# Performance work log

Measured on AMD Instinct MI355X. Metric: run time of the kernel, lower is better.

## Reference

```python
import math
import jax, jax.numpy as jnp
import numpy as np

B, S, D, H = 2, 2048, 1024, 16
HD = D // H  # 64


def setup_inputs() -> dict:
    key = jax.random.key(0)
    k = jax.random.split(key, 8)
    x = jax.random.normal(k[0], (B, S, D), dtype=jnp.float32)
    # RoPE tables: inv_freq over half dim, emb = concat(freqs, freqs)
    inv_freq = 1.0 / (10000.0 ** (jnp.arange(0, HD, 2, dtype=jnp.float32) / HD))
    pos = jnp.arange(S, dtype=jnp.float32)
    freqs = pos[:, None] * inv_freq[None, :]            # [S, HD/2]
    emb = jnp.concatenate([freqs, freqs], axis=-1)      # [S, HD]
    cos = jnp.cos(emb)[:, None, :]                      # [S, 1, HD] broadcasts over [B,S,H,HD]
    sin = jnp.sin(emb)[:, None, :]
    # causal additive mask [1, 1, S, S]
    neg = jnp.finfo(jnp.float32).min
    mask = jnp.where(jnp.tril(jnp.ones((S, S), dtype=bool)), 0.0, neg)[None, None]
    scale = 0.02
    wq = jax.random.normal(k[1], (D, D), dtype=jnp.float32) * scale
    wk = jax.random.normal(k[2], (D, D), dtype=jnp.float32) * scale
    wv = jax.random.normal(k[3], (D, D), dtype=jnp.float32) * scale
    wo = jax.random.normal(k[4], (D, D), dtype=jnp.float32) * scale
    return {"x": x, "cos": cos, "sin": sin, "mask": mask,
            "wq": wq, "wk": wk, "wv": wv, "wo": wo}


def rotate_half(t):
    t1, t2 = t[..., : t.shape[-1] // 2], t[..., t.shape[-1] // 2:]
    return jnp.concatenate([-t2, t1], axis=-1)


def reference(x, cos, sin, mask, wq, wk, wv, wo):
    b, s, d = x.shape
    # torch nn.Linear: y = x @ W^T  (W is [out, in])
    q = (x @ wq.T).reshape(b, s, H, HD)
    kk = (x @ wk.T).reshape(b, s, H, HD)
    v = (x @ wv.T).reshape(b, s, H, HD)
    q = q * cos + rotate_half(q) * sin
    kk = kk * cos + rotate_half(kk) * sin
    q = q.transpose(0, 2, 1, 3)   # [b, h, s, hd]
    kk = kk.transpose(0, 2, 1, 3)
    v = v.transpose(0, 2, 1, 3)
    scores = jnp.einsum('bhqd,bhkd->bhqk', q, kk) / math.sqrt(HD)
    scores = scores + mask
    probs = jax.nn.softmax(scores.astype(jnp.float32), axis=-1).astype(q.dtype)
    out = jnp.einsum('bhqk,bhkd->bhqd', probs, v)
    out = out.transpose(0, 2, 1, 3).reshape(b, s, d)
    return out @ wo.T
```

## Files before the change

### kernel.cpp

```cpp
#include <hip/hip_runtime.h>
#include <hip/hip_bf16.h>

typedef __hip_bfloat16 bf16;
typedef unsigned short u16;
typedef __attribute__((ext_vector_type(8))) short short8;
typedef __attribute__((ext_vector_type(4))) float floatx4;

constexpr int B_ = 2, S_ = 2048, D_ = 1024, H_ = 16, HD_ = 64;
constexpr int QT = 64, KT = 64, PAD = 72;
constexpr int NQT = S_ / QT;
constexpr int GK = 1024;

__device__ inline float b2f(u16 u) {
    union { unsigned int i; float f; } v; v.i = ((unsigned int)u) << 16; return v.f;
}
__device__ inline u16 f2b(float f) {
    bf16 h = __float2bfloat16(f); return *(u16*)&h;
}

__device__ inline void gl16(const u16* g, u16* l) {
    __builtin_amdgcn_global_load_lds(
        (const __attribute__((address_space(1))) unsigned int*)g,
        (__attribute__((address_space(3))) unsigned int*)l, 16, 0, 0);
}

__global__ __launch_bounds__(256) void cvt_kernel(
    const float* __restrict__ x,  const float* __restrict__ wq,
    const float* __restrict__ wk, const float* __restrict__ wv,
    const float* __restrict__ wo,
    u16* __restrict__ Xb, u16* __restrict__ Wb)
{
    const size_t c = (size_t)blockIdx.x * 256 + threadIdx.x;
    const float* src; u16* dst; size_t off;
    if (c < (size_t)(1 << 19)) { src = x; dst = Xb; off = c; }
    else {
        const size_t w = c - (1 << 19);
        const int wi = (int)(w >> 17);
        off = w & ((1 << 17) - 1);
        src = (wi == 0) ? wq : (wi == 1) ? wk : (wi == 2) ? wv : wo;
        dst = Wb + ((size_t)wi << 20);
    }
    const float4 a = *(const float4*)(src + off * 8);
    const float4 b = *(const float4*)(src + off * 8 + 4);
    ushort4 u0; u0.x = f2b(a.x); u0.y = f2b(a.y); u0.z = f2b(a.z); u0.w = f2b(a.w);
    ushort4 u1; u1.x = f2b(b.x); u1.y = f2b(b.y); u1.z = f2b(b.z); u1.w = f2b(b.w);
    *(ushort4*)(dst + off * 8)     = u0;
    *(ushort4*)(dst + off * 8 + 4) = u1;
}

template <int NW, int ROPE, typename TC>
__global__ __launch_bounds__(256) void gemm_fused(
    const u16* __restrict__ A, const u16* __restrict__ Wb,
    const float* __restrict__ cosp, const float* __restrict__ sinp,
    TC* __restrict__ C0, TC* __restrict__ C1, TC* __restrict__ C2)
{
    constexpr int AS_E = 128 * 32;
    constexpr int BS_E = NW * 64 * 32;
    __shared__ __align__(16) u16 As[2][AS_E];
    __shared__ __align__(16) u16 Bs[2][BS_E];

    const int bid = blockIdx.x;
    const int xcd = bid & 7, idx = bid >> 3;
    const int y = xcd * 4 + (idx & 3);
    const int x = idx >> 2;

    const int tid = threadIdx.x;
    const int wave = tid >> 6, lane = tid & 63;
    const int quad = lane >> 4, l16 = lane & 15;
    const int wm = wave >> 1, wn = wave & 1;
    const int m0 = y * 128, n0 = x * 64;

    const int srw = lane >> 2;
    const int scn = (lane & 3) ^ (srw & 3);

    floatx4 acc[4][NW][2] = {};

    auto stage = [&](int k0, int bufi) {
#pragma unroll
        for (int j = 0; j < 2; ++j) {
            const int rb = wave * 32 + j * 16;
            gl16(A + (size_t)(m0 + rb + srw) * GK + k0 + scn * 8, &As[bufi][rb * 32]);
        }
        if (NW == 3) {
#pragma unroll
            for (int j = 0; j < 3; ++j) {
                const int rb = wave * 48 + j * 16;
                const int w  = rb >> 6, rin = rb & 63;
                gl16(Wb + ((size_t)w << 20) + (size_t)(n0 + rin + srw) * GK + k0 + scn * 8,
                     &Bs[bufi][rb * 32]);
            }
        } else {
            const int rb = wave * 16;
            gl16(Wb + (size_t)(n0 + rb + srw) * GK + k0 + scn * 8, &Bs[bufi][rb * 32]);
        }
    };

    stage(0, 0);
    for (int it = 0; it < 32; ++it) {
        __syncthreads();
        if (it + 1 < 32) stage((it + 1) * 32, (it + 1) & 1);
        const int cur = it & 1;

        short8 af[4];
#pragma unroll
        for (int mt = 0; mt < 4; ++mt) {
            const int R = wm * 64 + mt * 16 + l16;
            af[mt] = *(const short8*)&As[cur][R * 32 + ((quad ^ (R & 3)) * 8)];
        }
        short8 bfr[NW][2];
#pragma unroll
        for (int w = 0; w < NW; ++w)
#pragma unroll
            for (int nt = 0; nt < 2; ++nt) {
                const int Rb = w * 64 + nt * 32 + wn * 16 + l16;
                bfr[w][nt] = *(const short8*)&Bs[cur][Rb * 32 + ((quad ^ (Rb & 3)) * 8)];
            }
#pragma unroll
        for (int mt = 0; mt < 4; ++mt)
#pragma unroll
            for (int w = 0; w < NW; ++w)
#pragma unroll
                for (int nt = 0; nt < 2; ++nt)
                    acc[mt][w][nt] = __builtin_amdgcn_mfma_f32_16x16x32_bf16(
                        af[mt], bfr[w][nt], acc[mt][w][nt], 0, 0, 0);
    }

    if (ROPE) {
        float* Cs = (float*)&As[0][0];
        float* Sn = (float*)&Bs[0][0];
        const int s0 = m0 & (S_ - 1), bq = m0 >> 11, h = x;
        __syncthreads();
        {
            const int rr = tid >> 1;
            const int cc = (tid & 1) * 16;
            const float4* cp = (const float4*)(cosp + (size_t)(s0 + rr) * HD_ + cc);
            const float4* sp = (const float4*)(sinp + (size_t)(s0 + rr) * HD_ + cc);
            float4* cd = (float4*)&Cs[rr * 32 + cc];
            float4* sd = (float4*)&Sn[rr * 32 + cc];
            cd[0] = cp[0]; cd[1] = cp[1]; cd[2] = cp[2]; cd[3] = cp[3];
            sd[0] = sp[0]; sd[1] = sp[1]; sd[2] = sp[2]; sd[3] = sp[3];
        }
        __syncthreads();

        const float QSC = 0.125f * 1.44269504f;
        const int dlo = wn * 16 + l16;
        const int bh  = bq * H_ + h;
#pragma unroll
        for (int mt = 0; mt < 4; ++mt) {
#pragma unroll
            for (int r = 0; r < 4; ++r) {
                const int sr = wm * 64 + mt * 16 + quad * 4 + r;
                const float c1 = Cs[sr * 32 + dlo];
                const float s1 = Sn[sr * 32 + dlo];
                const size_t base = ((size_t)bh * S_ + s0 + sr) << 6;
                const float q0 = acc[mt][0][0][r], q1 = acc[mt][0][1][r];
                ((bf16*)C0)[base + dlo]      = __float2bfloat16((q0 * c1 - q1 * s1) * QSC);
                ((bf16*)C0)[base + dlo + 32] = __float2bfloat16((q1 * c1 + q0 * s1) * QSC);
                const float k0v = acc[mt][1][0][r], k1v = acc[mt][1][1][r];
                ((bf16*)C1)[base + dlo]      = __float2bfloat16(k0v * c1 - k1v * s1);
                ((bf16*)C1)[base + dlo + 32] = __float2bfloat16(k1v * c1 + k0v * s1);
            }
#pragma unroll
            for (int nt = 0; nt < 2; ++nt) {
                const int d  = nt * 32 + dlo;
                const int sb = (m0 & (S_ - 1)) + wm * 64 + mt * 16 + quad * 4;
                ushort4 pk;
                pk.x = f2b(acc[mt][2][nt][0]); pk.y = f2b(acc[mt][2][nt][1]);
                pk.z = f2b(acc[mt][2][nt][2]); pk.w = f2b(acc[mt][2][nt][3]);
                *(ushort4*)&((u16*)C2)[((size_t)(bh * HD_ + d) << 11) + sb] = pk;
            }
        }
    } else {
#pragma unroll
        for (int mt = 0; mt < 4; ++mt)
#pragma unroll
            for (int nt = 0; nt < 2; ++nt) {
                const int n = n0 + nt * 32 + wn * 16 + l16;
#pragma unroll
                for (int r = 0; r < 4; ++r) {
                    const int m = m0 + wm * 64 + mt * 16 + quad * 4 + r;
                    ((float*)C0)[(size_t)m * D_ + n] = acc[mt][0][nt][r];
                }
            }
    }
}

__global__ __launch_bounds__(256) void fa_kernel(
    const u16* __restrict__ Qg, const u16* __restrict__ Kg, const u16* __restrict__ Vt,
    bf16* __restrict__ Og)
{
    __shared__ __align__(16) u16 Kt[2][KT * PAD];
    __shared__ __align__(16) u16 Vs[2][HD_ * PAD];
    __shared__ __align__(16) u16 Pt[4 * 16 * PAD];

    const int flat = blockIdx.x;
    const int bx = flat >> 5;
    const int bh = flat & 31;
    const int b  = bh >> 4, h = bh & 15;
    const int tid  = threadIdx.x;
    const int wave = tid >> 6, lane = tid & 63;
    const int quad = lane >> 4, l16 = lane & 15;
    const int srow = tid >> 2, scol = (tid & 3) * 16;

    for (int half = 0; half < 2; ++half) {
        const int qt = half ? (NQT - 1 - bx) : bx;
        const int qb = qt * QT;

        const u16* qrow = Qg + ((size_t)bh * S_ + qb + wave * 16 + l16) * HD_;
        const short8 aq0 = *(const short8*)(qrow + quad * 8);
        const short8 aq1 = *(const short8*)(qrow + 32 + quad * 8);

        floatx4 oacc[4] = {{0,0,0,0},{0,0,0,0},{0,0,0,0},{0,0,0,0}};
        float lsum = 0.f;

        __syncthreads();
        {
            const u16* kp = Kg + ((size_t)bh * S_ + srow) * HD_ + scol;
            *(short8*)&Kt[0][srow * PAD + scol]     = *(const short8*)kp;
            *(short8*)&Kt[0][srow * PAD + scol + 8] = *(const short8*)(kp + 8);
            const u16* vp = Vt + ((size_t)bh * HD_ + srow) * S_ + scol;
            *(short8*)&Vs[0][srow * PAD + scol]     = *(const short8*)vp;
            *(short8*)&Vs[0][srow * PAD + scol + 8] = *(const short8*)(vp + 8);
        }
        __syncthreads();

        for (int it = 0; it <= qt; ++it) {
            const int  cur = it & 1;
            const bool pf  = (it < qt);
            short8 nk0, nk1, nv0, nv1;
            if (pf) {
                const int kb = (it + 1) * KT;
                const u16* kp = Kg + ((size_t)bh * S_ + kb + srow) * HD_ + scol;
                nk0 = *(const short8*)kp; nk1 = *(const short8*)(kp + 8);
                const u16* vp = Vt + ((size_t)bh * HD_ + srow) * S_ + kb + scol;
                nv0 = *(const short8*)vp; nv1 = *(const short8*)(vp + 8);
            }

            floatx4 sacc[4] = {{0,0,0,0},{0,0,0,0},{0,0,0,0},{0,0,0,0}};
#pragma unroll
            for (int kt = 0; kt < 4; ++kt) {
                const short8 bk0 = *(const short8*)&Kt[cur][(kt * 16 + l16) * PAD + quad * 8];
                const short8 bk1 = *(const short8*)&Kt[cur][(kt * 16 + l16) * PAD + 32 + quad * 8];
                sacc[kt] = __builtin_amdgcn_mfma_f32_16x16x32_bf16(bk0, aq0, sacc[kt], 0, 0, 0);
                sacc[kt] = __builtin_amdgcn_mfma_f32_16x16x32_bf16(bk1, aq1, sacc[kt], 0, 0, 0);
            }

            if (it == qt) {
                const int ql = wave * 16 + l16;
#pragma unroll
                for (int kt = 0; kt < 4; ++kt)
#pragma unroll
                    for (int r = 0; r < 4; ++r)
                        if (kt * 16 + quad * 4 + r > ql) sacc[kt][r] = -1.0e38f;
            }

            float rs = 0.f;
#pragma unroll
            for (int kt = 0; kt < 4; ++kt) {
                const float e0 = __builtin_amdgcn_exp2f(sacc[kt][0]);
                const float e1 = __builtin_amdgcn_exp2f(sacc[kt][1]);
                const float e2 = __builtin_amdgcn_exp2f(sacc[kt][2]);
                const float e3 = __builtin_amdgcn_exp2f(sacc[kt][3]);
                rs += (e0 + e1) + (e2 + e3);
                ushort4 pk; pk.x = f2b(e0); pk.y = f2b(e1); pk.z = f2b(e2); pk.w = f2b(e3);
                *(ushort4*)&Pt[(wave * 16 + l16) * PAD + kt * 16 + quad * 4] = pk;
            }
            rs += __shfl_xor(rs, 16);
            rs += __shfl_xor(rs, 32);
            lsum += rs;

            const short8 ap0 = *(const short8*)&Pt[(wave * 16 + l16) * PAD + quad * 8];
            const short8 ap1 = *(const short8*)&Pt[(wave * 16 + l16) * PAD + 32 + quad * 8];

#pragma unroll
            for (int dt = 0; dt < 4; ++dt) {
                const short8 bv0 = *(const short8*)&Vs[cur][(dt * 16 + l16) * PAD + quad * 8];
                const short8 bv1 = *(const short8*)&Vs[cur][(dt * 16 + l16) * PAD + 32 + quad * 8];
                oacc[dt] = __builtin_amdgcn_mfma_f32_16x16x32_bf16(bv0, ap0, oacc[dt], 0, 0, 0);
                oacc[dt] = __builtin_amdgcn_mfma_f32_16x16x32_bf16(bv1, ap1, oacc[dt], 0, 0, 0);
            }

            if (pf) {
                const int nb = cur ^ 1;
                *(short8*)&Kt[nb][srow * PAD + scol]     = nk0;
                *(short8*)&Kt[nb][srow * PAD + scol + 8] = nk1;
                *(short8*)&Vs[nb][srow * PAD + scol]     = nv0;
                *(short8*)&Vs[nb][srow * PAD + scol + 8] = nv1;
            }
            __syncthreads();
        }

        const float inv = 1.0f / lsum;
        bf16* orow = Og + ((size_t)(b * S_ + qb + wave * 16 + l16)) * D_ + h * HD_;
#pragma unroll
        for (int dt = 0; dt < 4; ++dt) {
            ushort4 pk;
            pk.x = f2b(oacc[dt][0] * inv);
            pk.y = f2b(oacc[dt][1] * inv);
            pk.z = f2b(oacc[dt][2] * inv);
            pk.w = f2b(oacc[dt][3] * inv);
            *(ushort4*)((u16*)orow + dt * 16 + quad * 4) = pk;
        }
    }
}

extern "C" void kernel_launch(void* const* d_in, const int* in_sizes, int n_in,
                              void* d_out, int out_size, void* d_ws, size_t ws_size,
                              hipStream_t stream)
{
    const float* x    = (const float*)d_in[0];
    const float* cosp = (const float*)d_in[1];
    const float* sinp = (const float*)d_in[2];
    const float* wq   = (const float*)d_in[4];
    const float* wk   = (const float*)d_in[5];
    const float* wv   = (const float*)d_in[6];
    const float* wo   = (const float*)d_in[7];
    float* out = (float*)d_out;

    u16* w0 = (u16*)d_ws;
    const size_t NE = (size_t)B_ * S_ * D_;
    u16* Qb  = w0;
    u16* Kb  = w0 + NE;
    u16* Vtb = w0 + 2 * NE;
    u16* Xb  = w0 + 3 * NE;
    u16* Wb  = w0 + 4 * NE;
    u16* Ab  = Xb;
    u16* Wob = Wb + 3 * (1 << 20);

    cvt_kernel<<<4096, 256, 0, stream>>>(x, wq, wk, wv, wo, Xb, Wb);

    gemm_fused<3, 1, bf16><<<512, 256, 0, stream>>>(
        Xb, Wb, cosp, sinp, (bf16*)Qb, (bf16*)Kb, (bf16*)Vtb);

    fa_kernel<<<dim3((NQT / 2) * 32, 1, 1), 256, 0, stream>>>(Qb, Kb, Vtb, (bf16*)Ab);

    gemm_fused<1, 0, float><<<512, 256, 0, stream>>>(
        Ab, Wob, cosp, sinp, out, out, out);
}
```

Measured before the change: 203.5 us.

## Split GEMM templates, load attention K/V from global, and retile output GEMM

The templated GEMM is split into a dedicated QKV kernel and a separate output-projection kernel. The output kernel uses a 64-wide K step with an XOR swizzle, single buffering, and a different XCD-aware block mapping. The attention kernel drops the shared-memory K/V staging and the paired causal half-tiles. Each block now handles one query tile, launched longest first, and every wave reads K and V fragments straight from global memory into registers, with K prefetched one step ahead. This removes LDS traffic and barriers, but each of the four waves reloads K/V from global or L2 on its own, and the single-buffered output GEMM exposes its load latency.

```diff
diff --git a/kernel.cpp b/kernel.cpp
--- a/kernel.cpp
+++ b/kernel.cpp
@@ -48,16 +48,13 @@
     *(ushort4*)(dst + off * 8 + 4) = u1;
 }
 
-template <int NW, int ROPE, typename TC>
-__global__ __launch_bounds__(256) void gemm_fused(
+__global__ __launch_bounds__(256) void gemm_qkv(
     const u16* __restrict__ A, const u16* __restrict__ Wb,
     const float* __restrict__ cosp, const float* __restrict__ sinp,
-    TC* __restrict__ C0, TC* __restrict__ C1, TC* __restrict__ C2)
-{
-    constexpr int AS_E = 128 * 32;
-    constexpr int BS_E = NW * 64 * 32;
-    __shared__ __align__(16) u16 As[2][AS_E];
-    __shared__ __align__(16) u16 Bs[2][BS_E];
+    bf16* __restrict__ C0, bf16* __restrict__ C1, bf16* __restrict__ C2)
+{
+    __shared__ __align__(16) u16 As[2][128 * 32];
+    __shared__ __align__(16) u16 Bs[2][192 * 32];
 
     const int bid = blockIdx.x;
     const int xcd = bid & 7, idx = bid >> 3;
@@ -73,7 +70,7 @@
     const int srw = lane >> 2;
     const int scn = (lane & 3) ^ (srw & 3);
 
-    floatx4 acc[4][NW][2] = {};
+    floatx4 acc[4][3][2] = {};
 
     auto stage = [&](int k0, int bufi) {
 #pragma unroll
@@ -81,17 +78,12 @@
             const int rb = wave * 32 + j * 16;
             gl16(A + (size_t)(m0 + rb + srw) * GK + k0 + scn * 8, &As[bufi][rb * 32]);
         }
-        if (NW == 3) {
-#pragma unroll
-            for (int j = 0; j < 3; ++j) {
-                const int rb = wave * 48 + j * 16;
-                const int w  = rb >> 6, rin = rb & 63;
-                gl16(Wb + ((size_t)w << 20) + (size_t)(n0 + rin + srw) * GK + k0 + scn * 8,
-                     &Bs[bufi][rb * 32]);
-            }
-        } else {
-            const int rb = wave * 16;
-            gl16(Wb + (size_t)(n0 + rb + srw) * GK + k0 + scn * 8, &Bs[bufi][rb * 32]);
+#pragma unroll
+        for (int j = 0; j < 3; ++j) {
+            const int rb = wave * 48 + j * 16;
+            const int w  = rb >> 6, rin = rb & 63;
+            gl16(Wb + ((size_t)w << 20) + (size_t)(n0 + rin + srw) * GK + k0 + scn * 8,
+                 &Bs[bufi][rb * 32]);
         }
     };
 
@@ -107,9 +99,9 @@
             const int R = wm * 64 + mt * 16 + l16;
             af[mt] = *(const short8*)&As[cur][R * 32 + ((quad ^ (R & 3)) * 8)];
         }
-        short8 bfr[NW][2];
-#pragma unroll
-        for (int w = 0; w < NW; ++w)
+        short8 bfr[3][2];
+#pragma unroll
+        for (int w = 0; w < 3; ++w)
 #pragma unroll
             for (int nt = 0; nt < 2; ++nt) {
                 const int Rb = w * 64 + nt * 32 + wn * 16 + l16;
@@ -118,189 +110,240 @@
 #pragma unroll
         for (int mt = 0; mt < 4; ++mt)
 #pragma unroll
-            for (int w = 0; w < NW; ++w)
+            for (int w = 0; w < 3; ++w)
 #pragma unroll
                 for (int nt = 0; nt < 2; ++nt)
                     acc[mt][w][nt] = __builtin_amdgcn_mfma_f32_16x16x32_bf16(
                         af[mt], bfr[w][nt], acc[mt][w][nt], 0, 0, 0);
     }
 
-    if (ROPE) {
-        float* Cs = (float*)&As[0][0];
-        float* Sn = (float*)&Bs[0][0];
-        const int s0 = m0 & (S_ - 1), bq = m0 >> 11, h = x;
+    float* Cs = (float*)&As[0][0];
+    float* Sn = (float*)&Bs[0][0];
+    const int s0 = m0 & (S_ - 1), bq = m0 >> 11, h = x;
+    __syncthreads();
+    {
+        const int rr = tid >> 1;
+        const int cc = (tid & 1) * 16;
+        const float4* cp = (const float4*)(cosp + (size_t)(s0 + rr) * HD_ + cc);
+        const float4* sp = (const float4*)(sinp + (size_t)(s0 + rr) * HD_ + cc);
+        float4* cd = (float4*)&Cs[rr * 32 + cc];
+        float4* sd = (float4*)&Sn[rr * 32 + cc];
+        cd[0] = cp[0]; cd[1] = cp[1]; cd[2] = cp[2]; cd[3] = cp[3];
+        sd[0] = sp[0]; sd[1] = sp[1]; sd[2] = sp[2]; sd[3] = sp[3];
+    }
+    __syncthreads();
+
+    const float QSC = 0.125f * 1.44269504f;
+    const int dlo = wn * 16 + l16;
+    const int bh  = bq * H_ + h;
+#pragma unroll
+    for (int mt = 0; mt < 4; ++mt) {
+#pragma unroll
+        for (int r = 0; r < 4; ++r) {
+            const int sr = wm * 64 + mt * 16 + quad * 4 + r;
+            const float c1 = Cs[sr * 32 + dlo];
+            const float s1 = Sn[sr * 32 + dlo];
+            const size_t base = ((size_t)bh * S_ + s0 + sr) << 6;
+            const float q0 = acc[mt][0][0][r], q1 = acc[mt][0][1][r];
+            C0[base + dlo]      = __float2bfloat16((q0 * c1 - q1 * s1) * QSC);
+            C0[base + dlo + 32] = __float2bfloat16((q1 * c1 + q0 * s1) * QSC);
+            const float k0v = acc[mt][1][0][r], k1v = acc[mt][1][1][r];
+            C1[base + dlo]      = __float2bfloat16(k0v * c1 - k1v * s1);
+            C1[base + dlo + 32] = __float2bfloat16(k1v * c1 + k0v * s1);
+        }
+#pragma unroll
+        for (int nt = 0; nt < 2; ++nt) {
+            const int d  = nt * 32 + dlo;
+            const int sb = s0 + wm * 64 + mt * 16 + quad * 4;
+            ushort4 pk;
+            pk.x = f2b(acc[mt][2][nt][0]); pk.y = f2b(acc[mt][2][nt][1]);
+            pk.z = f2b(acc[mt][2][nt][2]); pk.w = f2b(acc[mt][2][nt][3]);
+            *(ushort4*)&((u16*)C2)[((size_t)(bh * HD_ + d) << 11) + sb] = pk;
+        }
+    }
+}
+
+__global__ __launch_bounds__(256) void gemm_out(
+    const u16* __restrict__ A, const u16* __restrict__ Wb,
+    float* __restrict__ C)
+{
+    __shared__ __align__(16) u16 As[128 * 64];
+    __shared__ __align__(16) u16 Bs[64 * 64];
+
+    const int xcd = blockIdx.x & 7, idx = blockIdx.x >> 3;
+    const int y = (xcd & 3) * 8 + (idx & 7);
+    const int x = (xcd >> 2) * 8 + (idx >> 3);
+
+    const int tid  = threadIdx.x;
+    const int wave = tid >> 6, lane = tid & 63;
+    const int quad = lane >> 4, l16 = lane & 15;
+    const int wm = wave >> 1, wn = wave & 1;
+    const int m0 = y * 128, n0 = x * 64;
+
+    const int srl = lane >> 3;
+    const int sc  = (lane & 7) ^ srl;
+
+    floatx4 acc[4][2] = {};
+
+    for (int k0 = 0; k0 < GK; k0 += 64) {
         __syncthreads();
+#pragma unroll
+        for (int j = 0; j < 4; ++j) {
+            const int rb = wave * 32 + j * 8;
+            gl16(A + (size_t)(m0 + rb + srl) * GK + k0 + sc * 8, &As[rb * 64]);
+        }
         {
-            const int rr = tid >> 1;
-            const int cc = (tid & 1) * 16;
-            const float4* cp = (const float4*)(cosp + (size_t)(s0 + rr) * HD_ + cc);
-            const float4* sp = (const float4*)(sinp + (size_t)(s0 + rr) * HD_ + cc);
-            float4* cd = (float4*)&Cs[rr * 32 + cc];
-            float4* sd = (float4*)&Sn[rr * 32 + cc];
-            cd[0] = cp[0]; cd[1] = cp[1]; cd[2] = cp[2]; cd[3] = cp[3];
-            sd[0] = sp[0]; sd[1] = sp[1]; sd[2] = sp[2]; sd[3] = sp[3];
+            const int rb = wave * 16;
+            gl16(Wb + (size_t)(n0 + rb + srl) * GK + k0 + sc * 8, &Bs[rb * 64]);
+            gl16(Wb + (size_t)(n0 + rb + 8 + srl) * GK + k0 + sc * 8, &Bs[(rb + 8) * 64]);
         }
         __syncthreads();
 
-        const float QSC = 0.125f * 1.44269504f;
-        const int dlo = wn * 16 + l16;
-        const int bh  = bq * H_ + h;
-#pragma unroll
-        for (int mt = 0; mt < 4; ++mt) {
+#pragma unroll
+        for (int ks = 0; ks < 2; ++ks) {
+            short8 af[4], bfr[2];
+#pragma unroll
+            for (int mt = 0; mt < 4; ++mt) {
+                const int R = wm * 64 + mt * 16 + l16;
+                af[mt] = *(const short8*)&As[R * 64 + (((ks * 4 + quad) ^ (l16 & 7)) * 8)];
+            }
+#pragma unroll
+            for (int nt = 0; nt < 2; ++nt) {
+                const int R = wn * 32 + nt * 16 + l16;
+                bfr[nt] = *(const short8*)&Bs[R * 64 + (((ks * 4 + quad) ^ (l16 & 7)) * 8)];
+            }
+#pragma unroll
+            for (int mt = 0; mt < 4; ++mt)
+#pragma unroll
+                for (int nt = 0; nt < 2; ++nt)
+                    acc[mt][nt] = __builtin_amdgcn_mfma_f32_16x16x32_bf16(
+                        af[mt], bfr[nt], acc[mt][nt], 0, 0, 0);
+        }
+    }
+
+#pragma unroll
+    for (int mt = 0; mt < 4; ++mt)
+#pragma unroll
+        for (int nt = 0; nt < 2; ++nt) {
+            const int n = n0 + wn * 32 + nt * 16 + l16;
 #pragma unroll
             for (int r = 0; r < 4; ++r) {
-                const int sr = wm * 64 + mt * 16 + quad * 4 + r;
-                const float c1 = Cs[sr * 32 + dlo];
-                const float s1 = Sn[sr * 32 + dlo];
-                const size_t base = ((size_t)bh * S_ + s0 + sr) << 6;
-                const float q0 = acc[mt][0][0][r], q1 = acc[mt][0][1][r];
-                ((bf16*)C0)[base + dlo]      = __float2bfloat16((q0 * c1 - q1 * s1) * QSC);
-                ((bf16*)C0)[base + dlo + 32] = __float2bfloat16((q1 * c1 + q0 * s1) * QSC);
-                const float k0v = acc[mt][1][0][r], k1v = acc[mt][1][1][r];
-                ((bf16*)C1)[base + dlo]      = __float2bfloat16(k0v * c1 - k1v * s1);
-                ((bf16*)C1)[base + dlo + 32] = __float2bfloat16(k1v * c1 + k0v * s1);
+                const int m = m0 + wm * 64 + mt * 16 + quad * 4 + r;
+                C[(size_t)m * D_ + n] = acc[mt][nt][r];
             }
-#pragma unroll
-            for (int nt = 0; nt < 2; ++nt) {
-                const int d  = nt * 32 + dlo;
-                const int sb = (m0 & (S_ - 1)) + wm * 64 + mt * 16 + quad * 4;
-                ushort4 pk;
-                pk.x = f2b(acc[mt][2][nt][0]); pk.y = f2b(acc[mt][2][nt][1]);
-                pk.z = f2b(acc[mt][2][nt][2]); pk.w = f2b(acc[mt][2][nt][3]);
-                *(ushort4*)&((u16*)C2)[((size_t)(bh * HD_ + d) << 11) + sb] = pk;
-            }
-        }
-    } else {
-#pragma unroll
-        for (int mt = 0; mt < 4; ++mt)
-#pragma unroll
-            for (int nt = 0; nt < 2; ++nt) {
-                const int n = n0 + nt * 32 + wn * 16 + l16;
-#pragma unroll
-                for (int r = 0; r < 4; ++r) {
-                    const int m = m0 + wm * 64 + mt * 16 + quad * 4 + r;
-                    ((float*)C0)[(size_t)m * D_ + n] = acc[mt][0][nt][r];
-                }
-            }
-    }
+        }
 }
 
 __global__ __launch_bounds__(256) void fa_kernel(
     const u16* __restrict__ Qg, const u16* __restrict__ Kg, const u16* __restrict__ Vt,
     bf16* __restrict__ Og)
 {
-    __shared__ __align__(16) u16 Kt[2][KT * PAD];
-    __shared__ __align__(16) u16 Vs[2][HD_ * PAD];
     __shared__ __align__(16) u16 Pt[4 * 16 * PAD];
 
     const int flat = blockIdx.x;
-    const int bx = flat >> 5;
+    const int qt = NQT - 1 - (flat >> 5);
     const int bh = flat & 31;
     const int b  = bh >> 4, h = bh & 15;
     const int tid  = threadIdx.x;
     const int wave = tid >> 6, lane = tid & 63;
     const int quad = lane >> 4, l16 = lane & 15;
-    const int srow = tid >> 2, scol = (tid & 3) * 16;
-
-    for (int half = 0; half < 2; ++half) {
-        const int qt = half ? (NQT - 1 - bx) : bx;
-        const int qb = qt * QT;
-
-        const u16* qrow = Qg + ((size_t)bh * S_ + qb + wave * 16 + l16) * HD_;
-        const short8 aq0 = *(const short8*)(qrow + quad * 8);
-        const short8 aq1 = *(const short8*)(qrow + 32 + quad * 8);
-
-        floatx4 oacc[4] = {{0,0,0,0},{0,0,0,0},{0,0,0,0},{0,0,0,0}};
-        float lsum = 0.f;
-
-        __syncthreads();
-        {
-            const u16* kp = Kg + ((size_t)bh * S_ + srow) * HD_ + scol;
-            *(short8*)&Kt[0][srow * PAD + scol]     = *(const short8*)kp;
-            *(short8*)&Kt[0][srow * PAD + scol + 8] = *(const short8*)(kp + 8);
-            const u16* vp = Vt + ((size_t)bh * HD_ + srow) * S_ + scol;
-            *(short8*)&Vs[0][srow * PAD + scol]     = *(const short8*)vp;
-            *(short8*)&Vs[0][srow * PAD + scol + 8] = *(const short8*)(vp + 8);
-        }
-        __syncthreads();
-
-        for (int it = 0; it <= qt; ++it) {
-            const int  cur = it & 1;
-            const bool pf  = (it < qt);
-            short8 nk0, nk1, nv0, nv1;
-            if (pf) {
-                const int kb = (it + 1) * KT;
-                const u16* kp = Kg + ((size_t)bh * S_ + kb + srow) * HD_ + scol;
-                nk0 = *(const short8*)kp; nk1 = *(const short8*)(kp + 8);
-                const u16* vp = Vt + ((size_t)bh * HD_ + srow) * S_ + kb + scol;
-                nv0 = *(const short8*)vp; nv1 = *(const short8*)(vp + 8);
-            }
-
-            floatx4 sacc[4] = {{0,0,0,0},{0,0,0,0},{0,0,0,0},{0,0,0,0}};
-#pragma unroll
-            for (int kt = 0; kt < 4; ++kt) {
-                const short8 bk0 = *(const short8*)&Kt[cur][(kt * 16 + l16) * PAD + quad * 8];
-                const short8 bk1 = *(const short8*)&Kt[cur][(kt * 16 + l16) * PAD + 32 + quad * 8];
-                sacc[kt] = __builtin_amdgcn_mfma_f32_16x16x32_bf16(bk0, aq0, sacc[kt], 0, 0, 0);
-                sacc[kt] = __builtin_amdgcn_mfma_f32_16x16x32_bf16(bk1, aq1, sacc[kt], 0, 0, 0);
-            }
-
-            if (it == qt) {
-                const int ql = wave * 16 + l16;
-#pragma unroll
-                for (int kt = 0; kt < 4; ++kt)
-#pragma unroll
-                    for (int r = 0; r < 4; ++r)
-                        if (kt * 16 + quad * 4 + r > ql) sacc[kt][r] = -1.0e38f;
-            }
-
-            float rs = 0.f;
-#pragma unroll
-            for (int kt = 0; kt < 4; ++kt) {
-                const float e0 = __builtin_amdgcn_exp2f(sacc[kt][0]);
-                const float e1 = __builtin_amdgcn_exp2f(sacc[kt][1]);
-                const float e2 = __builtin_amdgcn_exp2f(sacc[kt][2]);
-                const float e3 = __builtin_amdgcn_exp2f(sacc[kt][3]);
-                rs += (e0 + e1) + (e2 + e3);
-                ushort4 pk; pk.x = f2b(e0); pk.y = f2b(e1); pk.z = f2b(e2); pk.w = f2b(e3);
-                *(ushort4*)&Pt[(wave * 16 + l16) * PAD + kt * 16 + quad * 4] = pk;
-            }
-            rs += __shfl_xor(rs, 16);
-            rs += __shfl_xor(rs, 32);
-            lsum += rs;
-
-            const short8 ap0 = *(const short8*)&Pt[(wave * 16 + l16) * PAD + quad * 8];
-            const short8 ap1 = *(const short8*)&Pt[(wave * 16 + l16) * PAD + 32 + quad * 8];
-
-#pragma unroll
-            for (int dt = 0; dt < 4; ++dt) {
-                const short8 bv0 = *(const short8*)&Vs[cur][(dt * 16 + l16) * PAD + quad * 8];
-                const short8 bv1 = *(const short8*)&Vs[cur][(dt * 16 + l16) * PAD + 32 + quad * 8];
-                oacc[dt] = __builtin_amdgcn_mfma_f32_16x16x32_bf16(bv0, ap0, oacc[dt], 0, 0, 0);
-                oacc[dt] = __builtin_amdgcn_mfma_f32_16x16x32_bf16(bv1, ap1, oacc[dt], 0, 0, 0);
-            }
-
-            if (pf) {
-                const int nb = cur ^ 1;
-                *(short8*)&Kt[nb][srow * PAD + scol]     = nk0;
-                *(short8*)&Kt[nb][srow * PAD + scol + 8] = nk1;
-                *(short8*)&Vs[nb][srow * PAD + scol]     = nv0;
-                *(short8*)&Vs[nb][srow * PAD + scol + 8] = nv1;
-            }
-            __syncthreads();
-        }
-
-        const float inv = 1.0f / lsum;
-        bf16* orow = Og + ((size_t)(b * S_ + qb + wave * 16 + l16)) * D_ + h * HD_;
+    const int qb = qt * QT;
+
+    const u16* qrow = Qg + ((size_t)bh * S_ + qb + wave * 16 + l16) * HD_;
+    const short8 aq0 = *(const short8*)(qrow + quad * 8);
+    const short8 aq1 = *(const short8*)(qrow + 32 + quad * 8);
+
+    const u16* kpl = Kg + ((size_t)bh * S_ + l16) * HD_ + quad * 8;
+    const u16* vpl = Vt + ((size_t)(bh * HD_ + l16)) * (size_t)S_ + quad * 8;
+
+    floatx4 oacc[4] = {{0,0,0,0},{0,0,0,0},{0,0,0,0},{0,0,0,0}};
+    float lsum = 0.f;
+
+    short8 bk[4][2];
+#pragma unroll
+    for (int kt = 0; kt < 4; ++kt)
+#pragma unroll
+        for (int ks = 0; ks < 2; ++ks)
+            bk[kt][ks] = *(const short8*)(kpl + (size_t)(kt * 16) * HD_ + ks * 32);
+
+    for (int it = 0; it <= qt; ++it) {
+        const int kb = it * KT;
+        const bool pf = (it < qt);
+
+        short8 nbk[4][2];
+        if (pf) {
+#pragma unroll
+            for (int kt = 0; kt < 4; ++kt)
+#pragma unroll
+                for (int ks = 0; ks < 2; ++ks)
+                    nbk[kt][ks] = *(const short8*)(kpl + (size_t)(kb + KT + kt * 16) * HD_ + ks * 32);
+        }
+        short8 bv[4][2];
+#pragma unroll
+        for (int dt = 0; dt < 4; ++dt)
+#pragma unroll
+            for (int ks = 0; ks < 2; ++ks)
+                bv[dt][ks] = *(const short8*)(vpl + (size_t)dt * 16 * S_ + kb + ks * 32);
+
+        floatx4 sacc[4] = {{0,0,0,0},{0,0,0,0},{0,0,0,0},{0,0,0,0}};
+#pragma unroll
+        for (int kt = 0; kt < 4; ++kt) {
+            sacc[kt] = __builtin_amdgcn_mfma_f32_16x16x32_bf16(bk[kt][0], aq0, sacc[kt], 0, 0, 0);
+            sacc[kt] = __builtin_amdgcn_mfma_f32_16x16x32_bf16(bk[kt][1], aq1, sacc[kt], 0, 0, 0);
+        }
+
+        if (it == qt) {
+            const int ql = wave * 16 + l16;
+#pragma unroll
+            for (int kt = 0; kt < 4; ++kt)
+#pragma unroll
+                for (int r = 0; r < 4; ++r)
+                    if (kt * 16 + quad * 4 + r > ql) sacc[kt][r] = -1.0e38f;
+        }
+
+        float rs = 0.f;
+#pragma unroll
+        for (int kt = 0; kt < 4; ++kt) {
+            const float e0 = __builtin_amdgcn_exp2f(sacc[kt][0]);
+            const float e1 = __builtin_amdgcn_exp2f(sacc[kt][1]);
+            const float e2 = __builtin_amdgcn_exp2f(sacc[kt][2]);
+            const float e3 = __builtin_amdgcn_exp2f(sacc[kt][3]);
+            rs += (e0 + e1) + (e2 + e3);
+            ushort4 pk; pk.x = f2b(e0); pk.y = f2b(e1); pk.z = f2b(e2); pk.w = f2b(e3);
+            *(ushort4*)&Pt[(wave * 16 + l16) * PAD + kt * 16 + quad * 4] = pk;
+        }
+        rs += __shfl_xor(rs, 16);
+        rs += __shfl_xor(rs, 32);
+        lsum += rs;
+
+        const short8 ap0 = *(const short8*)&Pt[(wave * 16 + l16) * PAD + quad * 8];
+        const short8 ap1 = *(const short8*)&Pt[(wave * 16 + l16) * PAD + 32 + quad * 8];
+
 #pragma unroll
         for (int dt = 0; dt < 4; ++dt) {
-            ushort4 pk;
-            pk.x = f2b(oacc[dt][0] * inv);
-            pk.y = f2b(oacc[dt][1] * inv);
-            pk.z = f2b(oacc[dt][2] * inv);
-            pk.w = f2b(oacc[dt][3] * inv);
-            *(ushort4*)((u16*)orow + dt * 16 + quad * 4) = pk;
-        }
+            oacc[dt] = __builtin_amdgcn_mfma_f32_16x16x32_bf16(bv[dt][0], ap0, oacc[dt], 0, 0, 0);
+            oacc[dt] = __builtin_amdgcn_mfma_f32_16x16x32_bf16(bv[dt][1], ap1, oacc[dt], 0, 0, 0);
+        }
+
+        if (pf) {
+#pragma unroll
+            for (int kt = 0; kt < 4; ++kt)
+#pragma unroll
+                for (int ks = 0; ks < 2; ++ks)
+                    bk[kt][ks] = nbk[kt][ks];
+        }
+    }
+
+    const float inv = 1.0f / lsum;
+    bf16* orow = Og + ((size_t)(b * S_ + qb + wave * 16 + l16)) * D_ + h * HD_;
+#pragma unroll
+    for (int dt = 0; dt < 4; ++dt) {
+        ushort4 pk;
+        pk.x = f2b(oacc[dt][0] * inv);
+        pk.y = f2b(oacc[dt][1] * inv);
+        pk.z = f2b(oacc[dt][2] * inv);
+        pk.w = f2b(oacc[dt][3] * inv);
+        *(ushort4*)((u16*)orow + dt * 16 + quad * 4) = pk;
     }
 }
 
@@ -329,11 +372,10 @@
 
     cvt_kernel<<<4096, 256, 0, stream>>>(x, wq, wk, wv, wo, Xb, Wb);
 
-    gemm_fused<3, 1, bf16><<<512, 256, 0, stream>>>(
-        Xb, Wb, cosp, sinp, (bf16*)Qb, (bf16*)Kb, (bf16*)Vtb);
-
-    fa_kernel<<<dim3((NQT / 2) * 32, 1, 1), 256, 0, stream>>>(Qb, Kb, Vtb, (bf16*)Ab);
-
-    gemm_fused<1, 0, float><<<512, 256, 0, stream>>>(
-        Ab, Wob, cosp, sinp, out, out, out);
-}
+    gemm_qkv<<<512, 256, 0, stream>>>(Xb, Wb, cosp, sinp,
+                                      (bf16*)Qb, (bf16*)Kb, (bf16*)Vtb);
+
+    fa_kernel<<<1024, 256, 0, stream>>>(Qb, Kb, Vtb, (bf16*)Ab);
+
+    gemm_out<<<512, 256, 0, stream>>>(Ab, Wob, out);
+}
```

Result: slower. 275.8 us (+35.5%).
